# Kernel tuning notes

Hardware: AMD Instinct MI355X
Metric: run time of the kernel (lower is better)

The kernel has to match this reference:

```python
import jax, jax.numpy as jnp
import numpy as np

T = 16            # hardcoded timesteps in DQSN.forward
V_TH = 1.0        # IFNode default v_threshold
TAU = 2.0         # NonSpikingLIFNode tau
SG_ALPHA = 4.0    # spikingjelly surrogate.Sigmoid alpha


@jax.custom_vjp
def spike_fn(x):
    # Heaviside step with sigmoid surrogate gradient (spikingjelly default).
    return (x >= 0.0).astype(x.dtype)

def _spike_fwd(x):
    return spike_fn(x), x

def _spike_bwd(x, g):
    s = jax.nn.sigmoid(SG_ALPHA * x)
    return (g * SG_ALPHA * s * (1.0 - s),)

spike_fn.defvjp(_spike_fwd, _spike_bwd)


def setup_inputs() -> dict:
    key = jax.random.key(0)
    ks = jax.random.split(key, 5)
    B, H = 16384, 4096
    x = jax.random.normal(ks[0], (B, 4), dtype=jnp.float32)
    W1 = jax.random.normal(ks[1], (H, 4), dtype=jnp.float32) * 0.5   # Linear(4, H)
    b1 = jax.random.normal(ks[2], (H,), dtype=jnp.float32) * 0.1
    W2 = jax.random.normal(ks[3], (2, H), dtype=jnp.float32) * 0.02  # Linear(H, 2)
    b2 = jax.random.normal(ks[4], (2,), dtype=jnp.float32) * 0.1
    return {"x": x, "W1": W1, "b1": b1, "W2": W2, "b2": b2}


def reference(x, W1, b1, W2, b2):
    B = x.shape[0]
    H = W1.shape[0]
    # Input current is constant across the T steps (same x every step).
    I1 = x @ W1.T + b1                        # [B, H]

    def step(carry, _):
        v1, v2 = carry
        # IFNode: charge, spike (hard reset to v_reset=0)
        v1 = v1 + I1
        s = spike_fn(v1 - V_TH)               # [B, H]
        v1 = v1 * (1.0 - s)
        # Linear(H, 2) -> NonSpikingLIFNode: v += (dv - (v - 0)) / tau
        dv = s @ W2.T + b2                    # [B, 2]
        v2 = v2 + (dv - v2) / TAU
        return (v1, v2), None

    v1_0 = jnp.zeros((B, H), dtype=x.dtype)
    v2_0 = jnp.zeros((B, 2), dtype=x.dtype)
    (v1, v2), _ = jax.lax.scan(step, (v1_0, v2_0), None, length=T)
    return v2
```

## Files before the change

### kernel.cpp

```cpp
#include <hip/hip_runtime.h>


constexpr int TSTEPS = 16;
constexpr int NB = 8;
constexpr float GUARD = 4e-5f;

template <int CITERS>
__global__ __launch_bounds__(256) void dqsn_fwd(
    const float* __restrict__ x,
    const float* __restrict__ W1,
    const float* __restrict__ b1,
    const float* __restrict__ W2,
    const float* __restrict__ b2,
    float* __restrict__ out,
    int B, int H, int iters_rt)
{
    const int tid  = threadIdx.x;
    const int lane = tid & 63;
    const int b0   = blockIdx.x * NB;

    float tval = 0.0f;
    if (lane >= 1 && lane <= TSTEPS) {
        unsigned mm = 0;
        for (int k = lane; k <= TSTEPS; k += lane) mm |= 1u << (k - 1);
        tval = (float)mm * 0x1p-16f;
    }
    const int table_reg = __float_as_int(tval);

    float xs0[NB], xs1[NB], xs2[NB], xs3[NB];
#pragma unroll
    for (int i = 0; i < NB; ++i) {
        const int bi = (b0 + i < B) ? (b0 + i) : (B - 1);
        xs0[i] = x[bi * 4 + 0];
        xs1[i] = x[bi * 4 + 1];
        xs2[i] = x[bi * 4 + 2];
        xs3[i] = x[bi * 4 + 3];
    }

    float acc0[NB], acc1[NB];
#pragma unroll
    for (int i = 0; i < NB; ++i) { acc0[i] = 0.0f; acc1[i] = 0.0f; }

    const int iters = (CITERS > 0) ? CITERS : iters_rt;

#pragma unroll 4
    for (int it = 0; it < iters; ++it) {
        const int h = tid + (it << 8);
        const float4 w1 = *reinterpret_cast<const float4*>(W1 + (size_t)h * 4);
        const float bb  = b1[h];
        const float w2a = W2[h];
        const float w2b = W2[H + h];

        float I[NB];
        int   idx[NB];
        float e[NB];
#pragma unroll
        for (int i = 0; i < NB; ++i) {
            I[i] = fmaf(xs0[i], w1.x,
                   fmaf(xs1[i], w1.y,
                   fmaf(xs2[i], w1.z,
                   fmaf(xs3[i], w1.w, bb))));
            const float r = __builtin_amdgcn_rcpf(I[i]);
            const float c = __builtin_ceilf(r);
            const float m = __builtin_amdgcn_fmed3f(c, 0.0f, 17.0f);
            idx[i] = (int)m << 2;
            e[i] = (r - c) + 0.5f;
        }

        float g0 = fmaxf(fmaxf(fabsf(e[0]), fabsf(e[1])), fabsf(e[2]));
        float g1 = fmaxf(fmaxf(fabsf(e[3]), fabsf(e[4])), fabsf(e[5]));
        float g2 = fmaxf(fabsf(e[6]), fabsf(e[7]));
        const float gmax = fmaxf(fmaxf(g0, g1), g2);

        if (__builtin_expect((unsigned long long)__ballot(gmax > 0.5f - GUARD), 0)) {
#pragma unroll
            for (int i = 0; i < NB; ++i) {
                float v = 0.0f;
                int cnt = 0;
#pragma unroll
                for (int t = 0; t < TSTEPS; ++t) {
                    v += I[i];
                    cnt += (v < 1.0f) ? 1 : 0;
                }
                idx[i] = (cnt + 1 <= 16 ? cnt + 1 : 17) << 2;
            }
        }

#pragma unroll
        for (int i = 0; i < NB; ++i) {
            const float A = __int_as_float(__builtin_amdgcn_ds_bpermute(idx[i], table_reg));
            acc0[i] = fmaf(A, w2a, acc0[i]);
            acc1[i] = fmaf(A, w2b, acc1[i]);
        }
    }

#pragma unroll
    for (int i = 0; i < NB; ++i) {
#pragma unroll
        for (int off = 32; off > 0; off >>= 1) {
            acc0[i] += __shfl_xor(acc0[i], off, 64);
            acc1[i] += __shfl_xor(acc1[i], off, 64);
        }
    }

    __shared__ float red[4][NB][2];
    const int wave = tid >> 6;
    if ((tid & 63) == 0) {
#pragma unroll
        for (int i = 0; i < NB; ++i) {
            red[wave][i][0] = acc0[i];
            red[wave][i][1] = acc1[i];
        }
    }
    __syncthreads();

    if (tid < NB * 2) {
        const int i = tid >> 1;
        const int o = tid & 1;
        if (b0 + i < B) {
            const float s = ((red[0][i][o] + red[1][i][o]) +
                             (red[2][i][o] + red[3][i][o]))
                          + b2[o] * (1.0f - 0x1p-16f);
            out[(b0 + i) * 2 + o] = s;
        }
    }
}

extern "C" void kernel_launch(void* const* d_in, const int* in_sizes, int n_in,
                              void* d_out, int out_size, void* d_ws, size_t ws_size,
                              hipStream_t stream) {
    const float* x  = (const float*)d_in[0];
    const float* W1 = (const float*)d_in[1];
    const float* b1 = (const float*)d_in[2];
    const float* W2 = (const float*)d_in[3];
    const float* b2 = (const float*)d_in[4];
    float* out = (float*)d_out;

    const int B = in_sizes[0] / 4;
    const int H = in_sizes[2];

    const int grid = (B + NB - 1) / NB;
    if (H == 4096) {
        dqsn_fwd<16><<<grid, 256, 0, stream>>>(x, W1, b1, W2, b2, out, B, H, 16);
    } else {
        dqsn_fwd<0><<<grid, 256, 0, stream>>>(x, W1, b1, W2, b2, out, B, H, H / 256);
    }
}
```

Before: 39.77 us.

## Pack batch rows into float2 FMAs and use transpose-style wave reduction

Pairs of batch rows now share packed two-wide FMAs for the input current and the output accumulation, which targets the packed FP32 instructions. The table lookup is done eagerly, and the rare exact-simulation fallback adds a correction term instead of recomputing the index. The cross-lane reduction switches from 16 independent butterfly reductions to a recursive-halving transpose reduction that needs far fewer shuffles. It also fully unrolls the hidden loop and sets a launch-bounds occupancy hint, which may raise register pressure.

```diff
diff --git a/kernel.cpp b/kernel.cpp
--- a/kernel.cpp
+++ b/kernel.cpp
@@ -1,12 +1,16 @@
 #include <hip/hip_runtime.h>
 
+
+typedef float v2f __attribute__((ext_vector_type(2)));
 
 constexpr int TSTEPS = 16;
 constexpr int NB = 8;
+constexpr int NP = NB / 2;
 constexpr float GUARD = 4e-5f;
+constexpr float GTHR  = 0.5f - GUARD;
 
 template <int CITERS>
-__global__ __launch_bounds__(256) void dqsn_fwd(
+__global__ __launch_bounds__(256, 8) void dqsn_fwd(
     const float* __restrict__ x,
     const float* __restrict__ W1,
     const float* __restrict__ b1,
@@ -27,23 +31,28 @@
     }
     const int table_reg = __float_as_int(tval);
 
-    float xs0[NB], xs1[NB], xs2[NB], xs3[NB];
-#pragma unroll
-    for (int i = 0; i < NB; ++i) {
-        const int bi = (b0 + i < B) ? (b0 + i) : (B - 1);
-        xs0[i] = x[bi * 4 + 0];
-        xs1[i] = x[bi * 4 + 1];
-        xs2[i] = x[bi * 4 + 2];
-        xs3[i] = x[bi * 4 + 3];
-    }
-
-    float acc0[NB], acc1[NB];
-#pragma unroll
-    for (int i = 0; i < NB; ++i) { acc0[i] = 0.0f; acc1[i] = 0.0f; }
+    v2f xp0[NP], xp1[NP], xp2[NP], xp3[NP];
+#pragma unroll
+    for (int ip = 0; ip < NP; ++ip) {
+        int ra = b0 + 2 * ip, rb = b0 + 2 * ip + 1;
+        ra = (ra < B) ? ra : B - 1;
+        rb = (rb < B) ? rb : B - 1;
+        xp0[ip] = (v2f){x[ra * 4 + 0], x[rb * 4 + 0]};
+        xp1[ip] = (v2f){x[ra * 4 + 1], x[rb * 4 + 1]};
+        xp2[ip] = (v2f){x[ra * 4 + 2], x[rb * 4 + 2]};
+        xp3[ip] = (v2f){x[ra * 4 + 3], x[rb * 4 + 3]};
+    }
+
+    v2f acc0[NP], acc1[NP];
+#pragma unroll
+    for (int ip = 0; ip < NP; ++ip) {
+        acc0[ip] = (v2f){0.0f, 0.0f};
+        acc1[ip] = (v2f){0.0f, 0.0f};
+    }
 
     const int iters = (CITERS > 0) ? CITERS : iters_rt;
 
-#pragma unroll 4
+#pragma unroll
     for (int it = 0; it < iters; ++it) {
         const int h = tid + (it << 8);
         const float4 w1 = *reinterpret_cast<const float4*>(W1 + (size_t)h * 4);
@@ -51,78 +60,125 @@
         const float w2a = W2[h];
         const float w2b = W2[H + h];
 
-        float I[NB];
-        int   idx[NB];
-        float e[NB];
-#pragma unroll
-        for (int i = 0; i < NB; ++i) {
-            I[i] = fmaf(xs0[i], w1.x,
-                   fmaf(xs1[i], w1.y,
-                   fmaf(xs2[i], w1.z,
-                   fmaf(xs3[i], w1.w, bb))));
-            const float r = __builtin_amdgcn_rcpf(I[i]);
-            const float c = __builtin_ceilf(r);
-            const float m = __builtin_amdgcn_fmed3f(c, 0.0f, 17.0f);
-            idx[i] = (int)m << 2;
-            e[i] = (r - c) + 0.5f;
-        }
-
-        float g0 = fmaxf(fmaxf(fabsf(e[0]), fabsf(e[1])), fabsf(e[2]));
-        float g1 = fmaxf(fmaxf(fabsf(e[3]), fabsf(e[4])), fabsf(e[5]));
-        float g2 = fmaxf(fabsf(e[6]), fabsf(e[7]));
-        const float gmax = fmaxf(fmaxf(g0, g1), g2);
-
-        if (__builtin_expect((unsigned long long)__ballot(gmax > 0.5f - GUARD), 0)) {
-#pragma unroll
-            for (int i = 0; i < NB; ++i) {
-                float v = 0.0f;
-                int cnt = 0;
-#pragma unroll
-                for (int t = 0; t < TSTEPS; ++t) {
-                    v += I[i];
-                    cnt += (v < 1.0f) ? 1 : 0;
+        v2f I2[NP], Ap[NP];
+        float emax = 0.0f;
+#pragma unroll
+        for (int ip = 0; ip < NP; ++ip) {
+            v2f t  = __builtin_elementwise_fma(xp3[ip], (v2f){w1.w, w1.w}, (v2f){bb, bb});
+            t      = __builtin_elementwise_fma(xp2[ip], (v2f){w1.z, w1.z}, t);
+            t      = __builtin_elementwise_fma(xp1[ip], (v2f){w1.y, w1.y}, t);
+            I2[ip] = __builtin_elementwise_fma(xp0[ip], (v2f){w1.x, w1.x}, t);
+        }
+
+#pragma unroll
+        for (int ip = 0; ip < NP; ++ip) {
+            {
+                const float r = __builtin_amdgcn_rcpf(I2[ip].x);
+                const float c = __builtin_ceilf(r);
+                const int idx = (int)__builtin_amdgcn_fmed3f(c, 0.0f, 17.0f) << 2;
+                emax = fmaxf(emax, fabsf((r - c) + 0.5f));
+                Ap[ip].x = __int_as_float(__builtin_amdgcn_ds_bpermute(idx, table_reg));
+            }
+            {
+                const float r = __builtin_amdgcn_rcpf(I2[ip].y);
+                const float c = __builtin_ceilf(r);
+                const int idx = (int)__builtin_amdgcn_fmed3f(c, 0.0f, 17.0f) << 2;
+                emax = fmaxf(emax, fabsf((r - c) + 0.5f));
+                Ap[ip].y = __int_as_float(__builtin_amdgcn_ds_bpermute(idx, table_reg));
+            }
+        }
+
+#pragma unroll
+        for (int ip = 0; ip < NP; ++ip) {
+            acc0[ip] = __builtin_elementwise_fma(Ap[ip], (v2f){w2a, w2a}, acc0[ip]);
+            acc1[ip] = __builtin_elementwise_fma(Ap[ip], (v2f){w2b, w2b}, acc1[ip]);
+        }
+
+        if (__builtin_expect((unsigned long long)__ballot(emax > GTHR), 0)) {
+#pragma unroll
+            for (int ip = 0; ip < NP; ++ip) {
+#pragma unroll
+                for (int u = 0; u < 2; ++u) {
+                    const float I = u ? I2[ip].y : I2[ip].x;
+                    float v = 0.0f;
+                    int cnt = 0;
+#pragma unroll
+                    for (int t = 0; t < TSTEPS; ++t) {
+                        v += I;
+                        cnt += (v < 1.0f) ? 1 : 0;
+                    }
+                    const float An = __int_as_float(
+                        __builtin_amdgcn_ds_bpermute((cnt + 1) << 2, table_reg));
+                    const float Ao = u ? Ap[ip].y : Ap[ip].x;
+                    const float dA = An - Ao;
+                    if (u) {
+                        acc0[ip].y = fmaf(dA, w2a, acc0[ip].y);
+                        acc1[ip].y = fmaf(dA, w2b, acc1[ip].y);
+                    } else {
+                        acc0[ip].x = fmaf(dA, w2a, acc0[ip].x);
+                        acc1[ip].x = fmaf(dA, w2b, acc1[ip].x);
+                    }
                 }
-                idx[i] = (cnt + 1 <= 16 ? cnt + 1 : 17) << 2;
             }
         }
-
-#pragma unroll
-        for (int i = 0; i < NB; ++i) {
-            const float A = __int_as_float(__builtin_amdgcn_ds_bpermute(idx[i], table_reg));
-            acc0[i] = fmaf(A, w2a, acc0[i]);
-            acc1[i] = fmaf(A, w2b, acc1[i]);
-        }
-    }
-
-#pragma unroll
-    for (int i = 0; i < NB; ++i) {
-#pragma unroll
-        for (int off = 32; off > 0; off >>= 1) {
-            acc0[i] += __shfl_xor(acc0[i], off, 64);
-            acc1[i] += __shfl_xor(acc1[i], off, 64);
-        }
-    }
-
-    __shared__ float red[4][NB][2];
-    const int wave = tid >> 6;
-    if ((tid & 63) == 0) {
-#pragma unroll
-        for (int i = 0; i < NB; ++i) {
-            red[wave][i][0] = acc0[i];
-            red[wave][i][1] = acc1[i];
-        }
-    }
+    }
+
+    float v[16];
+#pragma unroll
+    for (int ip = 0; ip < NP; ++ip) {
+        v[4 * ip + 0] = acc0[ip].x;
+        v[4 * ip + 1] = acc1[ip].x;
+        v[4 * ip + 2] = acc0[ip].y;
+        v[4 * ip + 3] = acc1[ip].y;
+    }
+
+    {
+        const bool up = (lane & 32) != 0;
+#pragma unroll
+        for (int k = 0; k < 8; ++k) {
+            const float mine = up ? v[k] : v[k + 8];
+            const float recv = __shfl_xor(mine, 32, 64);
+            v[k] = (up ? v[k + 8] : v[k]) + recv;
+        }
+    }
+    {
+        const bool up = (lane & 16) != 0;
+#pragma unroll
+        for (int k = 0; k < 4; ++k) {
+            const float mine = up ? v[k] : v[k + 4];
+            const float recv = __shfl_xor(mine, 16, 64);
+            v[k] = (up ? v[k + 4] : v[k]) + recv;
+        }
+    }
+    {
+        const bool up = (lane & 8) != 0;
+#pragma unroll
+        for (int k = 0; k < 2; ++k) {
+            const float mine = up ? v[k] : v[k + 2];
+            const float recv = __shfl_xor(mine, 8, 64);
+            v[k] = (up ? v[k + 2] : v[k]) + recv;
+        }
+    }
+    {
+        const bool up = (lane & 4) != 0;
+        const float mine = up ? v[0] : v[1];
+        const float recv = __shfl_xor(mine, 4, 64);
+        v[0] = (up ? v[1] : v[0]) + recv;
+    }
+    float tot = v[0];
+    tot += __shfl_xor(tot, 1, 64);
+    tot += __shfl_xor(tot, 2, 64);
+
+    __shared__ float red[4][16];
+    if ((lane & 3) == 0) red[tid >> 6][lane >> 2] = tot;
     __syncthreads();
 
-    if (tid < NB * 2) {
+    if (tid < 16) {
+        const float s = (red[0][tid] + red[1][tid]) + (red[2][tid] + red[3][tid]);
         const int i = tid >> 1;
         const int o = tid & 1;
-        if (b0 + i < B) {
-            const float s = ((red[0][i][o] + red[1][i][o]) +
-                             (red[2][i][o] + red[3][i][o]))
-                          + b2[o] * (1.0f - 0x1p-16f);
-            out[(b0 + i) * 2 + o] = s;
-        }
+        if (b0 + i < B)
+            out[(b0 + i) * 2 + o] = s + b2[o] * (1.0f - 0x1p-16f);
     }
 }
 
```

New measurement: 38.23 us. -3.9%, faster.
